# Performance work log

Measured on AMD Instinct MI355X. Metric: run time of the kernel, lower is better.

## Reference

```python
import jax, jax.numpy as jnp
import numpy as np

R, T, N, OPS = 3, 3, 50000, 24
E, B, MAXDEG = 400000, 32, 8
QD, ED, H = 128, 128, 128


def lstm_scan(x, Wih, Whh, bih, bhh):
    # x: (T, B, D). PyTorch LSTM gate order: i, f, g, o.
    Hh = Whh.shape[-1]
    def step(carry, xt):
        h, c = carry
        g = xt @ Wih.T + bih + h @ Whh.T + bhh
        i, f, gg, o = jnp.split(g, 4, axis=-1)
        c = jax.nn.sigmoid(f) * c + jax.nn.sigmoid(i) * jnp.tanh(gg)
        h = jax.nn.sigmoid(o) * jnp.tanh(c)
        return (h, c), h
    z = jnp.zeros((x.shape[1], Hh), x.dtype)
    (hT, _), ys = jax.lax.scan(step, (z, z), x)
    return ys, hT


def bilstm(x, Wih, Whh, bih, bhh):
    # weights have a leading direction axis of size 2 (fwd, bwd)
    ys_f, h_f = lstm_scan(x, Wih[0], Whh[0], bih[0], bhh[0])
    ys_b, h_b = lstm_scan(x[::-1], Wih[1], Whh[1], bih[1], bhh[1])
    return jnp.concatenate([ys_f, ys_b[::-1]], -1), jnp.concatenate([h_f, h_b], -1)


def setup_inputs() -> dict:
    key = jax.random.key(0)
    ks = jax.random.split(key, 20)
    s = 0.05
    inp = {}
    inp["queries"] = jax.random.randint(ks[0], (B,), 0, OPS)
    inp["heads"] = jax.random.randint(ks[1], (B,), 0, N)
    inp["rels"] = jax.random.randint(ks[2], (E,), 0, OPS // 2)
    inp["t_heads"] = jax.random.randint(ks[3], (E,), 0, N)
    inp["t_tails"] = jax.random.randint(ks[4], (E,), 0, N)
    inp["entity_degrees"] = jax.random.randint(ks[5], (N, MAXDEG), 0, OPS + 1)
    inp["query_embedding"] = jax.random.normal(ks[6], (OPS, QD)) * s
    ent = jax.random.normal(ks[7], (OPS + 1, ED)) * s
    inp["entity_embedding"] = ent.at[OPS].set(0.0)  # padding_idx row is zero
    inp["q_Wih"] = jax.random.normal(ks[8], (R, 2, 4 * H, QD)) * s
    inp["q_Whh"] = jax.random.normal(ks[9], (R, 2, 4 * H, H)) * s
    inp["q_bih"] = jax.random.normal(ks[10], (R, 2, 4 * H)) * s
    inp["q_bhh"] = jax.random.normal(ks[11], (R, 2, 4 * H)) * s
    inp["e_Wih"] = jax.random.normal(ks[12], (2, 4 * H, ED)) * s
    inp["e_Whh"] = jax.random.normal(ks[13], (2, 4 * H, H)) * s
    inp["e_bih"] = jax.random.normal(ks[14], (2, 4 * H)) * s
    inp["e_bhh"] = jax.random.normal(ks[15], (2, 4 * H)) * s
    inp["q_lin_W"] = jax.random.normal(ks[16], (OPS + 1, 2 * H)) * s
    inp["q_lin_b"] = jax.random.normal(ks[17], (OPS + 1,)) * s
    inp["e_lin_W"] = jax.random.normal(ks[18], (OPS, 2 * H)) * s
    inp["e_lin_b"] = jax.random.normal(ks[19], (OPS,)) * s
    return inp


def reference(queries, heads, rels, t_heads, t_tails, entity_degrees,
              query_embedding, entity_embedding, q_Wih, q_Whh, q_bih, q_bhh,
              e_Wih, e_Whh, e_bih, e_bhh, q_lin_W, q_lin_b, e_lin_W, e_lin_b):
    # --- query attention over operators, one BiLSTM per rank ---
    qx = jnp.broadcast_to(query_embedding[queries][None], (T, B, QD))  # (T, B, QD)
    def q_branch(Wih, Whh, bih, bhh):
        ys, _ = bilstm(qx, Wih, Whh, bih, bhh)                 # (T, B, 2H)
        return jax.nn.softmax(ys @ q_lin_W.T + q_lin_b, axis=-1)  # (T, B, OPS+1)
    query_attn = jax.vmap(q_branch)(q_Wih, q_Whh, q_bih, q_bhh)   # (R, T, B, OPS+1)

    # --- entity attention from degree-sequence BiLSTM (final hidden states) ---
    ex = entity_embedding[entity_degrees].transpose(1, 0, 2)      # (MAXDEG, N, ED)
    _, e_h = bilstm(ex, e_Wih, e_Whh, e_bih, e_bhh)               # (N, 2H)
    entity_attn = jax.nn.softmax(e_h @ e_lin_W.T + e_lin_b, axis=-1)  # (N, OPS)

    # sparse operator values: A_rel[h, t] = entity_attn[h, rel] for fact (rel, h, t)
    w = entity_attn[t_heads, rels]  # (E,)
    half = OPS // 2

    logits = jnp.zeros((B, N), jnp.float32)
    for r in range(R):
        memory = jax.nn.one_hot(heads, N, dtype=jnp.float32)  # (B, N)
        for t in range(T):
            qa = query_attn[r, t]  # (B, OPS+1)
            # forward op: (memory @ A_rel), weighted by qa[rel]
            fwd = (qa[:, rels] * w[None, :]) * memory[:, t_heads]        # (B, E)
            # reverse op: (memory @ A_rel.T), weighted by qa[rel + half]
            rev = (qa[:, rels + half] * w[None, :]) * memory[:, t_tails]  # (B, E)
            added = (jnp.zeros((B, N), jnp.float32)
                     .at[:, t_tails].add(fwd)
                     .at[:, t_heads].add(rev))
            added = added + memory * qa[:, -1:]
            memory = added / jnp.maximum(1e-20, added.sum(axis=1, keepdims=True))
        logits = logits + memory
    return logits
```

## Files before the change

### kernel.cpp

```cpp
#include <hip/hip_runtime.h>

#define R_ 3
#define T_ 3
#define N_ 50000
#define OPS_ 24
#define E_ 400000
#define B_ 32
#define MAXDEG_ 8
#define QD_ 128
#define ED_ 128
#define H_ 128
#define G4_ (4*H_)
#define HPAD 168
#define PSLOTS 64
#define RB_ 96

#define QB_ (R_ * B_)
#define WB_ ((2*32*5*64*8 + 511) / 512)
#define CB_ ((E_ + 511) / 512)
#define BF_ ((E_ + 511) / 512)
#define ZU_ 586
#define ZM_ 25
#define ZS_ 12
#define EB_ 16
#define SCANBLK_ ((N_ + 31) / 32)

typedef unsigned short u16;
typedef unsigned char u8;
typedef __attribute__((ext_vector_type(8))) short bf16x8;
typedef __attribute__((ext_vector_type(8))) _Float16 f16x8;
typedef __attribute__((ext_vector_type(4))) float f32x4;

#define BF16_ONE ((short)0x3F80)
#define LOG2E_  1.44269504f
#define LOG2E2_ 2.88539008f

__device__ __forceinline__ short f2bf(float f){
  union { float f; unsigned u; } v; v.f = f;
  unsigned r = v.u + 0x7fffu + ((v.u >> 16) & 1u);
  return (short)(r >> 16);
}
__device__ __forceinline__ float bf2f(u16 u){
  union { unsigned u; float f; } v; v.u = ((unsigned)u) << 16; return v.f;
}
__device__ __forceinline__ float frcp(float x){ return __builtin_amdgcn_rcpf(x); }
__device__ __forceinline__ float fsig(float x){ return frcp(1.0f + __expf(-x)); }
__device__ __forceinline__ float ftanh(float x){
  return __builtin_fmaf(2.0f, fsig(2.0f * x), -1.0f);
}
__device__ __forceinline__ float fexp2(float x){
#if __has_builtin(__builtin_amdgcn_exp2f)
  return __builtin_amdgcn_exp2f(x);
#else
  return __expf(x * 0.6931471806f);
#endif
}

__device__ void qattn_body(int bid, const int* __restrict__ queries, const float* __restrict__ qemb,
    const float* __restrict__ qWih, const float* __restrict__ qWhh,
    const float* __restrict__ qbih, const float* __restrict__ qbhh,
    const float* __restrict__ qlinW, const float* __restrict__ qlinb,
    float* __restrict__ query_attn )
{
  int r = bid / B_;
  int b = bid % B_;
  int tid = threadIdx.x;
  int d   = tid >> 8;
  int t2  = tid & 255;
  __shared__ float x[QD_];
  __shared__ float gx[2][G4_];
  __shared__ float h[2][H_], c[2][H_];
  __shared__ float gtmp[2][G4_];
  __shared__ float hh[2][T_][H_];
  __shared__ float lg[OPS_ + 1];

  int q = queries[b];
  if (tid < QD_) x[tid] = qemb[q * QD_ + tid];
  __syncthreads();

  const float* Wih = qWih + (size_t)(r * 2 + d) * G4_ * QD_;
  const float* Whh = qWhh + (size_t)(r * 2 + d) * G4_ * H_;
  const float* bih = qbih + (r * 2 + d) * G4_;
  const float* bhh = qbhh + (r * 2 + d) * G4_;
  for (int j = t2; j < G4_; j += 256){
    const float4* wr = (const float4*)(Wih + (size_t)j * QD_);
    float s = bih[j] + bhh[j];
    for (int k = 0; k < QD_ / 4; ++k){
      float4 wv = wr[k];
      s += wv.x * x[4*k] + wv.y * x[4*k+1] + wv.z * x[4*k+2] + wv.w * x[4*k+3];
    }
    gx[d][j] = s;
  }
  if (t2 < H_){ h[d][t2] = 0.f; c[d][t2] = 0.f; }
  __syncthreads();
  for (int t = 0; t < T_; ++t){
    for (int j = t2; j < G4_; j += 256){
      const float4* wr = (const float4*)(Whh + (size_t)j * H_);
      float s = 0.f;
      for (int k = 0; k < H_ / 4; ++k){
        float4 wv = wr[k];
        s += wv.x * h[d][4*k] + wv.y * h[d][4*k+1] + wv.z * h[d][4*k+2] + wv.w * h[d][4*k+3];
      }
      gtmp[d][j] = gx[d][j] + s;
    }
    __syncthreads();
    if (t2 < H_){
      float gi = gtmp[d][t2], gf = gtmp[d][t2 + H_], gg = gtmp[d][t2 + 2*H_], go = gtmp[d][t2 + 3*H_];
      float cn = fsig(gf) * c[d][t2] + fsig(gi) * ftanh(gg);
      float hn = fsig(go) * ftanh(cn);
      c[d][t2] = cn; h[d][t2] = hn;
      hh[d][t][t2] = hn;
    }
    __syncthreads();
  }

  for (int t = 0; t < T_; ++t){
    if (tid < OPS_ + 1){
      const float* wr = qlinW + tid * (2 * H_);
      float s = qlinb[tid];
      for (int k = 0; k < H_; ++k) s += wr[k] * hh[0][t][k];
      for (int k = 0; k < H_; ++k) s += wr[H_ + k] * hh[1][T_ - 1 - t][k];
      lg[tid] = s;
    }
    __syncthreads();
    if (tid == 0){
      float m = -1e30f;
      for (int o = 0; o < OPS_ + 1; ++o) m = fmaxf(m, lg[o]);
      float sum = 0.f;
      for (int o = 0; o < OPS_ + 1; ++o){ float e = __expf(lg[o] - m); lg[o] = e; sum += e; }
      float inv = frcp(sum);
      for (int o = 0; o < OPS_ + 1; ++o) lg[o] *= inv;
    }
    __syncthreads();
    if (tid < OPS_ + 1) query_attn[((size_t)(r * T_ + t) * B_ + b) * (OPS_ + 1) + tid] = lg[tid];
    __syncthreads();
  }
}

__device__ void wbuild_body(int bid, const float* __restrict__ eWhh,
                            const float* __restrict__ eemb, const float* __restrict__ eWih,
                            const float* __restrict__ ebih, const float* __restrict__ ebhh,
                            u16* __restrict__ wtile, u16* __restrict__ wonehot)
{
  int idx = bid * 512 + threadIdx.x;
  if (idx >= 2 * 32 * 5 * 64 * 8) return;
  int jj = idx & 7;
  int lane = (idx >> 3) & 63;
  int kc = (idx >> 9) % 5;
  int gtile = (idx / (8 * 64 * 5)) & 31;
  int dir = idx / (8 * 64 * 5 * 32);
  int row = lane >> 4, col = lane & 15;
  int j = gtile * 16 + col;
  float sc = ((gtile >> 3) == 2) ? LOG2E2_ : LOG2E_;
  if (kc < 4){
    int k = kc * 32 + row * 8 + jj;
    float v = eWhh[((size_t)dir * G4_ + j) * H_ + k] * sc;
    wtile[((((size_t)dir * 32 + gtile) * 4 + kc) * 64 + lane) * 8 + jj] = (u16)f2bf(v);
  } else {
    int vdeg = row * 8 + jj;
    float v = 0.f;
    if (vdeg <= OPS_){
      const float4* wr = (const float4*)(eWih + (size_t)(dir * G4_ + j) * ED_);
      const float4* er = (const float4*)(eemb + (size_t)vdeg * ED_);
      float s = ebih[dir * G4_ + j] + ebhh[dir * G4_ + j];
      for (int k = 0; k < ED_ / 4; ++k){
        float4 wv = wr[k], ev = er[k];
        s += wv.x * ev.x + wv.y * ev.y + wv.z * ev.z + wv.w * ev.w;
      }
      v = s * sc;
    }
    wonehot[(((size_t)dir * 32 + gtile) * 64 + lane) * 8 + jj] = (u16)f2bf(v);
  }
}

__device__ void csr_count_body(int bid, const int* __restrict__ theads,
                               const int* __restrict__ ttails, int* __restrict__ counts)
{
  int e = bid * 512 + threadIdx.x;
  if (e < E_){
    atomicAdd(&counts[ttails[e]], 1);
    atomicAdd(&counts[theads[e]], 1);
  }
}

__device__ void bfs1_body(int bid, const int* __restrict__ heads,
                          const int* __restrict__ theads, const int* __restrict__ ttails,
                          u8* __restrict__ hs1)
{
  if (bid == 0 && threadIdx.x < B_) hs1[heads[threadIdx.x]] = 1;
  int e = bid * 512 + threadIdx.x;
  if (e < E_){
    int a = theads[e], t = ttails[e];
    #pragma unroll 8
    for (int i = 0; i < B_; ++i){
      int hd = heads[i];
      if (a == hd) hs1[t] = 1;
      if (t == hd) hs1[a] = 1;
    }
  }
}

__global__ __launch_bounds__(512) void front_kernel(
    const int* queries, const float* qemb,
    const float* qWih, const float* qWhh, const float* qbih, const float* qbhh,
    const float* qlinW, const float* qlinb, float* query_attn,
    const float* eWhh, const float* eemb, const float* eWih,
    const float* ebih, const float* ebhh, u16* wtile, u16* wonehot,
    const int* theads, const int* ttails, int* counts,
    const int* heads, u8* hs1,
    float* u2, int* maski, float* sumsP,
    const float* elinW, u16* etile)
{
  int bid = blockIdx.x;
  int tid = threadIdx.x;
  if (bid < QB_){
    qattn_body(bid, queries, qemb, qWih, qWhh, qbih, qbhh, qlinW, qlinb, query_attn);
  } else if (bid < QB_ + WB_){
    wbuild_body(bid - QB_, eWhh, eemb, eWih, ebih, ebhh, wtile, wonehot);
  } else if (bid < QB_ + WB_ + CB_){
    csr_count_body(bid - QB_ - WB_, theads, ttails, counts);
  } else if (bid < QB_ + WB_ + CB_ + BF_){
    bfs1_body(bid - QB_ - WB_ - CB_, heads, theads, ttails, hs1);
  } else if (bid < QB_ + WB_ + CB_ + BF_ + ZU_){
    int zb = bid - QB_ - WB_ - CB_ - BF_;
    float4 z = {0.f, 0.f, 0.f, 0.f};
    size_t base = (size_t)zb * 8192 + tid * 4;
    #pragma unroll
    for (int k = 0; k < 4; ++k){
      size_t idx = base + (size_t)k * 2048;
      if (idx < (size_t)N_ * RB_) *(float4*)&u2[idx] = z;
    }
  } else if (bid < QB_ + WB_ + CB_ + BF_ + ZU_ + ZM_){
    int mi = (bid - QB_ - WB_ - CB_ - BF_ - ZU_) * 512 + tid;
    if (mi < (N_ + 3) / 4) maski[mi] = 0;
  } else if (bid < QB_ + WB_ + CB_ + BF_ + ZU_ + ZM_ + ZS_){
    int si = (bid - QB_ - WB_ - CB_ - BF_ - ZU_ - ZM_) * 512 + tid;
    if (si < PSLOTS * RB_) sumsP[si] = 0.f;
  } else {
    int idx = (bid - (QB_ + WB_ + CB_ + BF_ + ZU_ + ZM_ + ZS_)) * 512 + tid;
    if (idx < 8192){
      int jj = idx & 7;
      int lane = (idx >> 3) & 63;
      int ks = (idx >> 9) & 7;
      int ot = idx >> 12;
      int op = ot * 16 + (lane & 15);
      int k  = ks * 32 + (lane >> 4) * 8 + jj;
      float v = (op < OPS_) ? elinW[(size_t)op * (2 * H_) + k] : 0.f;
      _Float16 hv = (_Float16)v;
      etile[idx] = *(const u16*)&hv;
    }
  }
}

__global__ __launch_bounds__(512) void bfs2_kernel(
    const int* __restrict__ theads, const int* __restrict__ ttails,
    const u8* __restrict__ hs1, u8* __restrict__ mask)
{
  int bid = blockIdx.x;
  if (bid < BF_){
    int e = bid * 512 + threadIdx.x;
    if (e < E_){
      int a = theads[e], t = ttails[e];
      if (hs1[a]) mask[t] = 1;
      if (hs1[t]) mask[a] = 1;
    }
  } else {
    int n = (bid - BF_) * 512 + threadIdx.x;
    if (n < N_ && hs1[n]) mask[n] = 1;
  }
}

__device__ void scan_body(const int* __restrict__ counts, int* __restrict__ rowptr,
                          int* __restrict__ cursor, int* __restrict__ cursor2)
{
  __shared__ int wsum[8];
  int t = threadIdx.x;
  int lane = t & 63, wv = t >> 6;
  int carry = 0;
  for (int base = 0; base < N_; base += 2048){
    int idx = base + t * 4;
    int c0 = 0, c1 = 0, c2 = 0, c3 = 0;
    if (idx + 3 < N_){
      int4 c = *(const int4*)&counts[idx];
      c0 = c.x; c1 = c.y; c2 = c.z; c3 = c.w;
    } else {
      if (idx     < N_) c0 = counts[idx];
      if (idx + 1 < N_) c1 = counts[idx + 1];
      if (idx + 2 < N_) c2 = counts[idx + 2];
      if (idx + 3 < N_) c3 = counts[idx + 3];
    }
    int s = c0 + c1 + c2 + c3;
    int sc = s;
    #pragma unroll
    for (int off = 1; off < 64; off <<= 1){
      int v = __shfl_up(sc, off);
      if (lane >= off) sc += v;
    }
    if (lane == 63) wsum[wv] = sc;
    __syncthreads();
    if (t == 0){
      int acc = carry;
      #pragma unroll
      for (int w = 0; w < 8; ++w){ int v = wsum[w]; wsum[w] = acc; acc += v; }
      carry = acc;
    }
    __syncthreads();
    int excl = wsum[wv] + (sc - s);
    int r0 = excl, r1 = r0 + c0, r2 = r1 + c1, r3 = r2 + c2;
    if (idx + 3 < N_){
      int4 rv; rv.x = r0; rv.y = r1; rv.z = r2; rv.w = r3;
      *(int4*)&rowptr[idx]  = rv;
      *(int4*)&cursor[idx]  = rv;
      *(int4*)&cursor2[idx] = rv;
    } else {
      if (idx     < N_){ rowptr[idx]   = r0; cursor[idx]   = r0; cursor2[idx]   = r0; }
      if (idx + 1 < N_){ rowptr[idx+1] = r1; cursor[idx+1] = r1; cursor2[idx+1] = r1; }
      if (idx + 2 < N_){ rowptr[idx+2] = r2; cursor[idx+2] = r2; cursor2[idx+2] = r2; }
      if (idx + 3 < N_){ rowptr[idx+3] = r3; cursor[idx+3] = r3; cursor2[idx+3] = r3; }
    }
  }
  if (t == 0) rowptr[N_] = carry;
}

__global__ __launch_bounds__(512, 4) void elstm_kernel(
    const int* __restrict__ degs,
    const u16* __restrict__ wtile, const u16* __restrict__ wonehot,
    const u16* __restrict__ etile, const float* __restrict__ elinb,
    float* __restrict__ attn ,
    const int* __restrict__ counts, int* __restrict__ rowptr,
    int* __restrict__ cursor, int* __restrict__ cursor2)
{
  if (blockIdx.x == 0){ scan_body(counts, rowptr, cursor, cursor2); return; }

  int tid = threadIdx.x;
  int lane = tid & 63;
  int w = tid >> 6;
  int wu = __builtin_amdgcn_readfirstlane(w);
  int row = lane >> 4, col = lane & 15;
  int ebase = (blockIdx.x - 1) * 32;

  __shared__ __align__(16) short hl[2][32 * HPAD];
  __shared__ __align__(16) short hfin[32 * 136];
  __shared__ float lgs[32][33];

  int eg0 = ebase + tid; if (eg0 >= N_) eg0 = N_ - 1;

  for (int i = tid; i < 2 * 32 * HPAD; i += 512) ((short*)hl)[i] = 0;
  __syncthreads();
  if (tid < 32) hl[0][tid * HPAD + H_ + degs[(size_t)eg0 * MAXDEG_ + 0]] = BF16_ONE;
  __syncthreads();

  int swzr = (col >> 2) & 3;

  for (int dir = 0; dir < 2; ++dir){
    const u16* Wt  = wtile   + (size_t)dir * 32 * 4 * 64 * 8;
    const u16* Woh = wonehot + (size_t)dir * 32 * 64 * 8;
    const u16* W0 = Wt + (size_t)((0 * 8 + wu) * 4 * 64) * 8;
    const u16* W1 = Wt + (size_t)((1 * 8 + wu) * 4 * 64) * 8;
    const u16* W2 = Wt + (size_t)((2 * 8 + wu) * 4 * 64) * 8;
    const u16* W3 = Wt + (size_t)((3 * 8 + wu) * 4 * 64) * 8;
    const u16* O0 = Woh + (size_t)((0 * 8 + wu) * 64) * 8;
    const u16* O1 = Woh + (size_t)((1 * 8 + wu) * 64) * 8;
    const u16* O2 = Woh + (size_t)((2 * 8 + wu) * 64) * 8;
    const u16* O3 = Woh + (size_t)((3 * 8 + wu) * 64) * 8;
    float cst[8];
    #pragma unroll
    for (int i = 0; i < 8; ++i) cst[i] = 0.f;

    for (int t = 0; t < MAXDEG_; ++t){
      const short* hb = hl[t & 1];
      short*       hw = hl[(t + 1) & 1];
      f32x4 acc[8];
      #pragma unroll
      for (int i = 0; i < 8; ++i) acc[i] = (f32x4){0.f, 0.f, 0.f, 0.f};

      #pragma unroll 2
      for (int kc = 0; kc < 4; ++kc){
        bf16x8 af0 = *(const bf16x8*)&hb[(col) * HPAD + kc * 32 + (row ^ swzr) * 8];
        bf16x8 af1 = *(const bf16x8*)&hb[(16 + col) * HPAD + kc * 32 + (row ^ swzr) * 8];
        int lo = (kc * 64 + lane) * 8;
        bf16x8 b0 = *(const bf16x8*)(W0 + lo);
        bf16x8 b1 = *(const bf16x8*)(W1 + lo);
        bf16x8 b2 = *(const bf16x8*)(W2 + lo);
        bf16x8 b3 = *(const bf16x8*)(W3 + lo);
        acc[0] = __builtin_amdgcn_mfma_f32_16x16x32_bf16(af0, b0, acc[0], 0, 0, 0);
        acc[1] = __builtin_amdgcn_mfma_f32_16x16x32_bf16(af1, b0, acc[1], 0, 0, 0);
        acc[2] = __builtin_amdgcn_mfma_f32_16x16x32_bf16(af0, b1, acc[2], 0, 0, 0);
        acc[3] = __builtin_amdgcn_mfma_f32_16x16x32_bf16(af1, b1, acc[3], 0, 0, 0);
        acc[4] = __builtin_amdgcn_mfma_f32_16x16x32_bf16(af0, b2, acc[4], 0, 0, 0);
        acc[5] = __builtin_amdgcn_mfma_f32_16x16x32_bf16(af1, b2, acc[5], 0, 0, 0);
        acc[6] = __builtin_amdgcn_mfma_f32_16x16x32_bf16(af0, b3, acc[6], 0, 0, 0);
        acc[7] = __builtin_amdgcn_mfma_f32_16x16x32_bf16(af1, b3, acc[7], 0, 0, 0);
      }
      {
        bf16x8 af0 = *(const bf16x8*)&hb[(col) * HPAD + H_ + row * 8];
        bf16x8 af1 = *(const bf16x8*)&hb[(16 + col) * HPAD + H_ + row * 8];
        int lo = lane * 8;
        bf16x8 b0 = *(const bf16x8*)(O0 + lo);
        bf16x8 b1 = *(const bf16x8*)(O1 + lo);
        bf16x8 b2 = *(const bf16x8*)(O2 + lo);
        bf16x8 b3 = *(const bf16x8*)(O3 + lo);
        acc[0] = __builtin_amdgcn_mfma_f32_16x16x32_bf16(af0, b0, acc[0], 0, 0, 0);
        acc[1] = __builtin_amdgcn_mfma_f32_16x16x32_bf16(af1, b0, acc[1], 0, 0, 0);
        acc[2] = __builtin_amdgcn_mfma_f32_16x16x32_bf16(af0, b1, acc[2], 0, 0, 0);
        acc[3] = __builtin_amdgcn_mfma_f32_16x16x32_bf16(af1, b1, acc[3], 0, 0, 0);
        acc[4] = __builtin_amdgcn_mfma_f32_16x16x32_bf16(af0, b2, acc[4], 0, 0, 0);
        acc[5] = __builtin_amdgcn_mfma_f32_16x16x32_bf16(af1, b2, acc[5], 0, 0, 0);
        acc[6] = __builtin_amdgcn_mfma_f32_16x16x32_bf16(af0, b3, acc[6], 0, 0, 0);
        acc[7] = __builtin_amdgcn_mfma_f32_16x16x32_bf16(af1, b3, acc[7], 0, 0, 0);
      }

      #pragma unroll
      for (int mt = 0; mt < 2; ++mt){
        #pragma unroll
        for (int reg = 0; reg < 4; ++reg){
          int e = mt * 16 + row * 4 + reg;
          int jsw = (((wu * 2 + (col >> 3)) ^ row) * 8) + (col & 7);
          float Gi = acc[0 + mt][reg];
          float Gf = acc[2 + mt][reg];
          float Gg = acc[4 + mt][reg];
          float Go = acc[6 + mt][reg];
          int ci = mt * 4 + reg;
          float ea = fexp2(-Gi);
          float ef = fexp2(-Gf);
          float eb = fexp2(-Gg);
          float eo = fexp2(-Go);
          float t1 = 1.f + ef, t2 = 1.f + ea, t3 = 1.f + eb;
          float p = t2 * t3;
          float num = __builtin_fmaf(cst[ci], p, (1.f - eb) * t1);
          float cn = num * frcp(t1 * p);
          float ed = fexp2(cn * (-LOG2E2_));
          float hn = (1.f - ed) * frcp((1.f + eo) * (1.f + ed));
          cst[ci] = cn;
          hw[e * HPAD + jsw] = f2bf(hn);
        }
      }
      if (tid < 32){
        const int* dr = degs + (size_t)eg0 * MAXDEG_;
        if (t >= 1)
          hw[tid * HPAD + H_ + dr[dir ? (MAXDEG_ - t) : (t - 1)]] = 0;
        if (t < MAXDEG_ - 1)
          hw[tid * HPAD + H_ + dr[dir ? (MAXDEG_ - 2 - t) : (t + 1)]] = BF16_ONE;
      }
      __syncthreads();
    }

    if (dir == 0){
      for (int i = tid; i < 32 * 16; i += 512){
        int e = i >> 4, c = i & 15;
        int sz = (e >> 2) & 3;
        *(bf16x8*)&hfin[e * 136 + c * 8] =
            *(const bf16x8*)&hl[0][e * HPAD + ((c ^ sz) * 8)];
      }
      __syncthreads();
      for (int i = tid; i < 2 * 32 * HPAD; i += 512) ((short*)hl)[i] = 0;
      __syncthreads();
      if (tid < 32) hl[0][tid * HPAD + H_ + degs[(size_t)eg0 * MAXDEG_ + (MAXDEG_ - 1)]] = BF16_ONE;
      __syncthreads();
    }
  }

  if (wu < 4){
    int mt = wu >> 1, ot = wu & 1;
    int e2 = mt * 16 + col;
    f32x4 accL = (f32x4){0.f, 0.f, 0.f, 0.f};
    #pragma unroll
    for (int ks = 0; ks < 8; ++ks){
      bf16x8 ra;
      if (ks < 4) ra = *(const bf16x8*)&hfin[e2 * 136 + ks * 32 + row * 8];
      else        ra = *(const bf16x8*)&hl[0][e2 * HPAD + (ks - 4) * 32 + (row ^ swzr) * 8];
      f16x8 af;
      #pragma unroll
      for (int jj = 0; jj < 8; ++jj) af[jj] = (_Float16)bf2f((u16)ra[jj]);
      f16x8 bfr = *(const f16x8*)(etile + (((size_t)(ot * 8 + ks)) * 64 + lane) * 8);
      accL = __builtin_amdgcn_mfma_f32_16x16x32_f16(af, bfr, accL, 0, 0, 0);
    }
    #pragma unroll
    for (int reg = 0; reg < 4; ++reg){
      int ent = mt * 16 + (lane >> 4) * 4 + reg;
      int op  = ot * 16 + (lane & 15);
      float bb = (op < OPS_) ? elinb[op] : 0.f;
      lgs[ent][op] = accL[reg] + bb;
    }
  }
  __syncthreads();
  if (tid < 32){
    int n = ebase + tid;
    if (n < N_){
      float m = -1e30f;
      #pragma unroll
      for (int o = 0; o < OPS_; ++o) m = fmaxf(m, lgs[tid][o]);
      float s = 0.f;
      #pragma unroll
      for (int o = 0; o < OPS_; ++o) s += __expf(lgs[tid][o] - m);
      float inv = frcp(s);
      #pragma unroll
      for (int o = 0; o < OPS_; ++o)
        attn[(size_t)n * OPS_ + o] = __expf(lgs[tid][o] - m) * inv;
    }
  }
}

__global__ void csr_fill_kernel(const int* __restrict__ rels, const int* __restrict__ theads,
                                const int* __restrict__ ttails, const float* __restrict__ attn,
                                const u8* __restrict__ mask, const u8* __restrict__ hs1,
                                int* __restrict__ cursor, int* __restrict__ cursor2,
                                uint2* __restrict__ ents, uint2* __restrict__ ents2)
{
  int e = blockIdx.x * 256 + threadIdx.x;
  if (e < E_){
    int hh = theads[e], tt = ttails[e];
    int mh = mask[hh], mt = mask[tt];
    if (!(mh | mt)) return;
    int rel = rels[e];
    unsigned wb = __float_as_uint(attn[(size_t)hh * OPS_ + rel]);
    if (mh){
      uint2 v1; v1.x = (unsigned)hh | ((unsigned)rel << 16); v1.y = wb;
      ents[atomicAdd(&cursor[tt], 1)] = v1;
    }
    if (mt){
      uint2 v2; v2.x = (unsigned)tt | ((unsigned)(rel + OPS_/2) << 16); v2.y = wb;
      ents[atomicAdd(&cursor[hh], 1)] = v2;
    }
    if (hs1[hh]){
      uint2 w1; w1.x = (unsigned)tt | ((unsigned)rel << 16); w1.y = wb;
      ents2[atomicAdd(&cursor2[hh], 1)] = w1;
    }
    if (hs1[tt]){
      uint2 w2; w2.x = (unsigned)hh | ((unsigned)(rel + OPS_/2) << 16); w2.y = wb;
      ents2[atomicAdd(&cursor2[tt], 1)] = w2;
    }
  }
}

__global__ void t01_kernel(const int* __restrict__ heads, const float* __restrict__ query_attn,
                           const int* __restrict__ rowptr, const int* __restrict__ cend2,
                           const uint2* __restrict__ ents2, float* __restrict__ u2)
{
  __shared__ float qa0[OPS_ + 1], qa1[OPS_ + 1];
  int blk = blockIdx.x;
  int r = blk >> 5, b = blk & 31;
  int rb = r * 32 + b;
  int tid = threadIdx.x;
  if (tid < OPS_ + 1){
    qa0[tid] = query_attn[((size_t)(r * T_ + 0) * B_ + b) * (OPS_ + 1) + tid];
    qa1[tid] = query_attn[((size_t)(r * T_ + 1) * B_ + b) * (OPS_ + 1) + tid];
  }
  __syncthreads();
  int hd = heads[b];
  int beg = rowptr[hd], end = cend2[hd];
  float q024 = qa0[OPS_], q124 = qa1[OPS_];
  if (tid == 0) atomicAdd(&u2[(size_t)hd * RB_ + rb], q124 * q024);
  for (int i = beg + tid; i < end; i += 64){
    uint2 e1 = ents2[i];
    int s  = (int)(e1.x & 0xFFFFu);
    int r1 = (int)(e1.x >> 16);
    float w1 = __uint_as_float(e1.y);
    atomicAdd(&u2[(size_t)s * RB_ + rb], w1 * (q124 * qa0[r1] + qa1[r1] * q024));
    float v1 = qa0[r1] * w1;
    int b2 = rowptr[s], e2e = cend2[s];
    for (int jj = b2; jj < e2e; ++jj){
      uint2 e2 = ents2[jj];
      int d2 = (int)(e2.x & 0xFFFFu);
      int r2 = (int)(e2.x >> 16);
      atomicAdd(&u2[(size_t)d2 * RB_ + rb], qa1[r2] * __uint_as_float(e2.y) * v1);
    }
  }
}

__global__ __launch_bounds__(256) void gather3_kernel(
    const float* __restrict__ ucur, float* __restrict__ unxt,
    const float* __restrict__ query_attn, int t,
    const int* __restrict__ rowptr, const int* __restrict__ cend,
    const uint2* __restrict__ ents, const u8* __restrict__ mask,
    float* __restrict__ partial )
{
  __shared__ float qas[3 * B_ * (OPS_ + 1)];
  __shared__ float red[RB_];
  int tid = threadIdx.x;
  for (int i = tid; i < 3 * B_ * (OPS_ + 1); i += 256){
    int r = i / (B_ * (OPS_ + 1));
    int rem = i - r * (B_ * (OPS_ + 1));
    qas[i] = query_attn[(size_t)(r * T_ + t) * B_ * (OPS_ + 1) + rem];
  }
  if (tid < RB_) red[tid] = 0.f;
  __syncthreads();
  int b  = tid & 31;
  int h  = (tid >> 5) & 1;
  int n = blockIdx.x * 4 + (tid >> 6);
  const float* q0 = &qas[0 * 800 + b * (OPS_ + 1)];
  const float* q1 = &qas[1 * 800 + b * (OPS_ + 1)];
  const float* q2 = &qas[2 * 800 + b * (OPS_ + 1)];
  size_t nb = (size_t)n * RB_;
  float a0 = 0.f, a1 = 0.f, a2 = 0.f;
  if (h == 0 && mask[n]){
    a0 = ucur[nb + b]      * q0[OPS_];
    a1 = ucur[nb + 32 + b] * q1[OPS_];
    a2 = ucur[nb + 64 + b] * q2[OPS_];
  }
  int beg = rowptr[n], end = cend[n];
  int cnt = end - beg;
  int nq = cnt >> 2;
  for (int c = h; c < nq; c += 2){
    int i0 = beg + 4 * c;
    uint2 e0 = ents[i0 + 0];
    uint2 e1 = ents[i0 + 1];
    uint2 e2 = ents[i0 + 2];
    uint2 e3 = ents[i0 + 3];
    size_t s0 = (size_t)(e0.x & 0xFFFFu) * RB_;
    size_t s1 = (size_t)(e1.x & 0xFFFFu) * RB_;
    size_t s2 = (size_t)(e2.x & 0xFFFFu) * RB_;
    size_t s3 = (size_t)(e3.x & 0xFFFFu) * RB_;
    float u00 = ucur[s0 + b], u01 = ucur[s0 + 32 + b], u02 = ucur[s0 + 64 + b];
    float u10 = ucur[s1 + b], u11 = ucur[s1 + 32 + b], u12 = ucur[s1 + 64 + b];
    float u20 = ucur[s2 + b], u21 = ucur[s2 + 32 + b], u22 = ucur[s2 + 64 + b];
    float u30 = ucur[s3 + b], u31 = ucur[s3 + 32 + b], u32 = ucur[s3 + 64 + b];
    int r0 = (int)(e0.x >> 16), r1 = (int)(e1.x >> 16);
    int r2 = (int)(e2.x >> 16), r3 = (int)(e3.x >> 16);
    float w0 = __uint_as_float(e0.y), w1 = __uint_as_float(e1.y);
    float w2 = __uint_as_float(e2.y), w3 = __uint_as_float(e3.y);
    a0 += q0[r0]*w0*u00 + q0[r1]*w1*u10 + q0[r2]*w2*u20 + q0[r3]*w3*u30;
    a1 += q1[r0]*w0*u01 + q1[r1]*w1*u11 + q1[r2]*w2*u21 + q1[r3]*w3*u31;
    a2 += q2[r0]*w0*u02 + q2[r1]*w1*u12 + q2[r2]*w2*u22 + q2[r3]*w3*u32;
  }
  if (h == 1){
    for (int i = beg + 4 * nq; i < end; ++i){
      uint2 e0 = ents[i];
      size_t s0 = (size_t)(e0.x & 0xFFFFu) * RB_;
      int r0 = (int)(e0.x >> 16);
      float w0 = __uint_as_float(e0.y);
      a0 += q0[r0] * w0 * ucur[s0 + b];
      a1 += q1[r0] * w0 * ucur[s0 + 32 + b];
      a2 += q2[r0] * w0 * ucur[s0 + 64 + b];
    }
  }
  a0 += __shfl_xor(a0, 32);
  a1 += __shfl_xor(a1, 32);
  a2 += __shfl_xor(a2, 32);
  if (h == 0){
    unxt[nb + b]      = a0;
    unxt[nb + 32 + b] = a1;
    unxt[nb + 64 + b] = a2;
    atomicAdd(&red[b], a0);
    atomicAdd(&red[32 + b], a1);
    atomicAdd(&red[64 + b], a2);
  }
  __syncthreads();
  if (tid < RB_)
    atomicAdd(&partial[(blockIdx.x & (PSLOTS - 1)) * RB_ + tid], red[tid]);
}

__global__ void fintrans_kernel(const float* __restrict__ u, const float* __restrict__ partial,
                                float* __restrict__ out)
{
  __shared__ float sinv[RB_];
  __shared__ float t[B_][72];
  int tid = threadIdx.x;
  if (tid < RB_){
    float s = 0.f;
    #pragma unroll 8
    for (int k = 0; k < PSLOTS; ++k) s += partial[k * RB_ + tid];
    sinv[tid] = frcp(fmaxf(1e-20f, s));
  }
  __syncthreads();
  int n0 = blockIdx.x * 64;
  for (int i = tid; i < 64 * B_; i += 256){
    int nl = i >> 5, b = i & 31;
    int n = n0 + nl;
    float v = 0.f;
    if (n < N_){
      size_t nb = (size_t)n * RB_;
      v = u[nb + b] * sinv[b] + u[nb + 32 + b] * sinv[32 + b] + u[nb + 64 + b] * sinv[64 + b];
    }
    t[b][nl] = v;
  }
  __syncthreads();
  for (int i = tid; i < 64 * B_; i += 256){
    int b = i >> 6, nl = i & 63;
    int n = n0 + nl;
    if (n < N_) out[(size_t)b * N_ + n] = t[b][nl];
  }
}

extern "C" void kernel_launch(void* const* d_in, const int* in_sizes, int n_in,
                              void* d_out, int out_size, void* d_ws, size_t ws_size,
                              hipStream_t stream)
{
  const int*   queries = (const int*)d_in[0];
  const int*   heads   = (const int*)d_in[1];
  const int*   rels    = (const int*)d_in[2];
  const int*   t_heads = (const int*)d_in[3];
  const int*   t_tails = (const int*)d_in[4];
  const int*   edeg    = (const int*)d_in[5];
  const float* qemb    = (const float*)d_in[6];
  const float* eemb    = (const float*)d_in[7];
  const float* qWih    = (const float*)d_in[8];
  const float* qWhh    = (const float*)d_in[9];
  const float* qbih    = (const float*)d_in[10];
  const float* qbhh    = (const float*)d_in[11];
  const float* eWih    = (const float*)d_in[12];
  const float* eWhh    = (const float*)d_in[13];
  const float* ebih    = (const float*)d_in[14];
  const float* ebhh    = (const float*)d_in[15];
  const float* qlinW   = (const float*)d_in[16];
  const float* qlinb   = (const float*)d_in[17];
  const float* elinW   = (const float*)d_in[18];
  const float* elinb   = (const float*)d_in[19];
  float* out = (float*)d_out;

  char* ws = (char*)d_ws;
  size_t off = 0;
  auto alloc = [&](size_t bytes){ void* p = ws + off; off += (bytes + 255) & ~(size_t)255; return p; };
  char*  bigB  = (char*)alloc((size_t)N_ * RB_ * 4);
  float* attn  = (float*)bigB;
  float* u3    = (float*)bigB;
  uint2* ents       = (uint2*)alloc((size_t)2 * E_ * 8);
  float* u2         = (float*)alloc((size_t)N_ * RB_ * 4);
  uint2* ents2      = (uint2*)alloc((size_t)2 * E_ * 8);
  float* query_attn = (float*)alloc((size_t)R_ * T_ * B_ * (OPS_ + 1) * 4);
  u16*   wtile      = (u16*)  alloc((size_t)2 * 32 * 4 * 64 * 8 * 2);
  u16*   wonehot    = (u16*)  alloc((size_t)2 * 32 * 64 * 8 * 2);
  u16*   etile      = (u16*)  alloc((size_t)2 * 8 * 64 * 8 * 2);
  int*   counts     = (int*)  alloc((size_t)(N_ + 1) * 4);
  int*   rowptr     = (int*)  alloc((size_t)(N_ + 1) * 4);
  int*   cursor     = (int*)  alloc((size_t)(N_ + 1) * 4);
  int*   cursor2    = (int*)  alloc((size_t)(N_ + 1) * 4);
  u8*    hs1        = (u8*)   alloc((size_t)N_);
  u8*    mask       = (u8*)   alloc((size_t)N_);
  float* sumsP      = (float*)alloc((size_t)PSLOTS * RB_ * 4);

  hipMemsetAsync(counts, 0, (size_t)(N_ + 1) * 4, stream);
  hipMemsetAsync(hs1, 0, (size_t)N_, stream);

  front_kernel<<<QB_ + WB_ + CB_ + BF_ + ZU_ + ZM_ + ZS_ + EB_, 512, 0, stream>>>(
      queries, qemb, qWih, qWhh, qbih, qbhh, qlinW, qlinb, query_attn,
      eWhh, eemb, eWih, ebih, ebhh, wtile, wonehot,
      t_heads, t_tails, counts, heads, hs1, u2, (int*)mask, sumsP, elinW, etile);
  bfs2_kernel<<<BF_ + (N_ + 511) / 512, 512, 0, stream>>>(t_heads, t_tails, hs1, mask);
  elstm_kernel<<<SCANBLK_ + 1, 512, 0, stream>>>(edeg, wtile, wonehot, etile, elinb,
                                                 attn, counts, rowptr, cursor, cursor2);
  csr_fill_kernel<<<(E_ + 255) / 256, 256, 0, stream>>>(rels, t_heads, t_tails, attn,
                                                        mask, hs1, cursor, cursor2,
                                                        ents, ents2);
  t01_kernel<<<RB_, 64, 0, stream>>>(heads, query_attn, rowptr, cursor2, ents2, u2);
  gather3_kernel<<<N_ / 4, 256, 0, stream>>>(u2, u3, query_attn, 2, rowptr, cursor,
                                             ents, mask, sumsP);
  fintrans_kernel<<<(N_ + 63) / 64, 256, 0, stream>>>(u3, sumsP, out);
}
```

Before: 463.2 us.

## Fold bfs2 and query-attention blocks into elstm launch; skip empty gather nodes

Removes the separate bfs2 launch and moves the query-attention LSTM blocks out of front_kernel into extra blocks of elstm_kernel alongside the scan block. This cuts one kernel launch and shortens front_kernel's critical path. gather3 now lets whole blocks exit early when all four nodes have no edges and no mask bit, and it skips writing their u3 values. fintrans reads zero for those nodes instead of the unwritten u3. The price is a block-wide sync before the shared-memory load and extra index reads in fintrans.

```diff
diff --git a/kernel.cpp b/kernel.cpp
--- a/kernel.cpp
+++ b/kernel.cpp
@@ -15,7 +15,6 @@
 #define PSLOTS 64
 #define RB_ 96
 
-#define QB_ (R_ * B_)
 #define WB_ ((2*32*5*64*8 + 511) / 512)
 #define CB_ ((E_ + 511) / 512)
 #define BF_ ((E_ + 511) / 512)
@@ -23,6 +22,11 @@
 #define ZM_ 25
 #define ZS_ 12
 #define EB_ 16
+
+#define QB_ (R_ * B_)
+#define BF2E_ ((E_ + 511) / 512)
+#define BF2N_ ((N_ + 511) / 512)
+#define RIDERS_ (1 + BF2E_ + BF2N_ + QB_)
 #define SCANBLK_ ((N_ + 31) / 32)
 
 typedef unsigned short u16;
@@ -201,9 +205,6 @@
 }
 
 __global__ __launch_bounds__(512) void front_kernel(
-    const int* queries, const float* qemb,
-    const float* qWih, const float* qWhh, const float* qbih, const float* qbhh,
-    const float* qlinW, const float* qlinb, float* query_attn,
     const float* eWhh, const float* eemb, const float* eWih,
     const float* ebih, const float* ebhh, u16* wtile, u16* wonehot,
     const int* theads, const int* ttails, int* counts,
@@ -213,16 +214,14 @@
 {
   int bid = blockIdx.x;
   int tid = threadIdx.x;
-  if (bid < QB_){
-    qattn_body(bid, queries, qemb, qWih, qWhh, qbih, qbhh, qlinW, qlinb, query_attn);
-  } else if (bid < QB_ + WB_){
-    wbuild_body(bid - QB_, eWhh, eemb, eWih, ebih, ebhh, wtile, wonehot);
-  } else if (bid < QB_ + WB_ + CB_){
-    csr_count_body(bid - QB_ - WB_, theads, ttails, counts);
-  } else if (bid < QB_ + WB_ + CB_ + BF_){
-    bfs1_body(bid - QB_ - WB_ - CB_, heads, theads, ttails, hs1);
-  } else if (bid < QB_ + WB_ + CB_ + BF_ + ZU_){
-    int zb = bid - QB_ - WB_ - CB_ - BF_;
+  if (bid < WB_){
+    wbuild_body(bid, eWhh, eemb, eWih, ebih, ebhh, wtile, wonehot);
+  } else if (bid < WB_ + CB_){
+    csr_count_body(bid - WB_, theads, ttails, counts);
+  } else if (bid < WB_ + CB_ + BF_){
+    bfs1_body(bid - WB_ - CB_, heads, theads, ttails, hs1);
+  } else if (bid < WB_ + CB_ + BF_ + ZU_){
+    int zb = bid - WB_ - CB_ - BF_;
     float4 z = {0.f, 0.f, 0.f, 0.f};
     size_t base = (size_t)zb * 8192 + tid * 4;
     #pragma unroll
@@ -230,14 +229,14 @@
       size_t idx = base + (size_t)k * 2048;
       if (idx < (size_t)N_ * RB_) *(float4*)&u2[idx] = z;
     }
-  } else if (bid < QB_ + WB_ + CB_ + BF_ + ZU_ + ZM_){
-    int mi = (bid - QB_ - WB_ - CB_ - BF_ - ZU_) * 512 + tid;
+  } else if (bid < WB_ + CB_ + BF_ + ZU_ + ZM_){
+    int mi = (bid - WB_ - CB_ - BF_ - ZU_) * 512 + tid;
     if (mi < (N_ + 3) / 4) maski[mi] = 0;
-  } else if (bid < QB_ + WB_ + CB_ + BF_ + ZU_ + ZM_ + ZS_){
-    int si = (bid - QB_ - WB_ - CB_ - BF_ - ZU_ - ZM_) * 512 + tid;
+  } else if (bid < WB_ + CB_ + BF_ + ZU_ + ZM_ + ZS_){
+    int si = (bid - WB_ - CB_ - BF_ - ZU_ - ZM_) * 512 + tid;
     if (si < PSLOTS * RB_) sumsP[si] = 0.f;
   } else {
-    int idx = (bid - (QB_ + WB_ + CB_ + BF_ + ZU_ + ZM_ + ZS_)) * 512 + tid;
+    int idx = (bid - (WB_ + CB_ + BF_ + ZU_ + ZM_ + ZS_)) * 512 + tid;
     if (idx < 8192){
       int jj = idx & 7;
       int lane = (idx >> 3) & 63;
@@ -252,12 +251,11 @@
   }
 }
 
-__global__ __launch_bounds__(512) void bfs2_kernel(
-    const int* __restrict__ theads, const int* __restrict__ ttails,
-    const u8* __restrict__ hs1, u8* __restrict__ mask)
-{
-  int bid = blockIdx.x;
-  if (bid < BF_){
+__device__ void bfs2_body(int bid, const int* __restrict__ theads,
+                          const int* __restrict__ ttails,
+                          const u8* __restrict__ hs1, u8* __restrict__ mask)
+{
+  if (bid < BF2E_){
     int e = bid * 512 + threadIdx.x;
     if (e < E_){
       int a = theads[e], t = ttails[e];
@@ -265,7 +263,7 @@
       if (hs1[t]) mask[a] = 1;
     }
   } else {
-    int n = (bid - BF_) * 512 + threadIdx.x;
+    int n = (bid - BF2E_) * 512 + threadIdx.x;
     if (n < N_ && hs1[n]) mask[n] = 1;
   }
 }
@@ -328,16 +326,30 @@
     const u16* __restrict__ etile, const float* __restrict__ elinb,
     float* __restrict__ attn ,
     const int* __restrict__ counts, int* __restrict__ rowptr,
-    int* __restrict__ cursor, int* __restrict__ cursor2)
-{
-  if (blockIdx.x == 0){ scan_body(counts, rowptr, cursor, cursor2); return; }
+    int* __restrict__ cursor, int* __restrict__ cursor2,
+    const int* __restrict__ theads, const int* __restrict__ ttails,
+    const u8* __restrict__ hs1, u8* __restrict__ mask,
+    const int* __restrict__ queries, const float* __restrict__ qemb,
+    const float* __restrict__ qWih, const float* __restrict__ qWhh,
+    const float* __restrict__ qbih, const float* __restrict__ qbhh,
+    const float* __restrict__ qlinW, const float* __restrict__ qlinb,
+    float* __restrict__ query_attn)
+{
+  int bid = blockIdx.x;
+  if (bid == 0){ scan_body(counts, rowptr, cursor, cursor2); return; }
+  if (bid < 1 + BF2E_ + BF2N_){ bfs2_body(bid - 1, theads, ttails, hs1, mask); return; }
+  if (bid < RIDERS_){
+    qattn_body(bid - (1 + BF2E_ + BF2N_), queries, qemb, qWih, qWhh, qbih, qbhh,
+               qlinW, qlinb, query_attn);
+    return;
+  }
 
   int tid = threadIdx.x;
   int lane = tid & 63;
   int w = tid >> 6;
   int wu = __builtin_amdgcn_readfirstlane(w);
   int row = lane >> 4, col = lane & 15;
-  int ebase = (blockIdx.x - 1) * 32;
+  int ebase = (bid - RIDERS_) * 32;
 
   __shared__ __align__(16) short hl[2][32 * HPAD];
   __shared__ __align__(16) short hfin[32 * 136];
@@ -578,6 +590,14 @@
   __shared__ float qas[3 * B_ * (OPS_ + 1)];
   __shared__ float red[RB_];
   int tid = threadIdx.x;
+  int b  = tid & 31;
+  int h  = (tid >> 5) & 1;
+  int n = blockIdx.x * 4 + (tid >> 6);
+  int beg = rowptr[n], end = cend[n];
+  int mk = mask[n];
+  int cnt = end - beg;
+  if (__syncthreads_and(cnt == 0 && !mk)) return;
+
   for (int i = tid; i < 3 * B_ * (OPS_ + 1); i += 256){
     int r = i / (B_ * (OPS_ + 1));
     int rem = i - r * (B_ * (OPS_ + 1));
@@ -585,21 +605,16 @@
   }
   if (tid < RB_) red[tid] = 0.f;
   __syncthreads();
-  int b  = tid & 31;
-  int h  = (tid >> 5) & 1;
-  int n = blockIdx.x * 4 + (tid >> 6);
   const float* q0 = &qas[0 * 800 + b * (OPS_ + 1)];
   const float* q1 = &qas[1 * 800 + b * (OPS_ + 1)];
   const float* q2 = &qas[2 * 800 + b * (OPS_ + 1)];
   size_t nb = (size_t)n * RB_;
   float a0 = 0.f, a1 = 0.f, a2 = 0.f;
-  if (h == 0 && mask[n]){
+  if (h == 0 && mk){
     a0 = ucur[nb + b]      * q0[OPS_];
     a1 = ucur[nb + 32 + b] * q1[OPS_];
     a2 = ucur[nb + 64 + b] * q2[OPS_];
   }
-  int beg = rowptr[n], end = cend[n];
-  int cnt = end - beg;
   int nq = cnt >> 2;
   for (int c = h; c < nq; c += 2){
     int i0 = beg + 4 * c;
@@ -637,7 +652,7 @@
   a0 += __shfl_xor(a0, 32);
   a1 += __shfl_xor(a1, 32);
   a2 += __shfl_xor(a2, 32);
-  if (h == 0){
+  if (h == 0 && (mk || cnt > 0)){
     unxt[nb + b]      = a0;
     unxt[nb + 32 + b] = a1;
     unxt[nb + 64 + b] = a2;
@@ -651,6 +666,8 @@
 }
 
 __global__ void fintrans_kernel(const float* __restrict__ u, const float* __restrict__ partial,
+                                const int* __restrict__ rowptr, const int* __restrict__ cend,
+                                const u8* __restrict__ mask,
                                 float* __restrict__ out)
 {
   __shared__ float sinv[RB_];
@@ -668,7 +685,7 @@
     int nl = i >> 5, b = i & 31;
     int n = n0 + nl;
     float v = 0.f;
-    if (n < N_){
+    if (n < N_ && (mask[n] || cend[n] > rowptr[n])){
       size_t nb = (size_t)n * RB_;
       v = u[nb + b] * sinv[b] + u[nb + 32 + b] * sinv[32 + b] + u[nb + 64 + b] * sinv[64 + b];
     }
@@ -732,18 +749,20 @@
   hipMemsetAsync(counts, 0, (size_t)(N_ + 1) * 4, stream);
   hipMemsetAsync(hs1, 0, (size_t)N_, stream);
 
-  front_kernel<<<QB_ + WB_ + CB_ + BF_ + ZU_ + ZM_ + ZS_ + EB_, 512, 0, stream>>>(
-      queries, qemb, qWih, qWhh, qbih, qbhh, qlinW, qlinb, query_attn,
+  front_kernel<<<WB_ + CB_ + BF_ + ZU_ + ZM_ + ZS_ + EB_, 512, 0, stream>>>(
       eWhh, eemb, eWih, ebih, ebhh, wtile, wonehot,
       t_heads, t_tails, counts, heads, hs1, u2, (int*)mask, sumsP, elinW, etile);
-  bfs2_kernel<<<BF_ + (N_ + 511) / 512, 512, 0, stream>>>(t_heads, t_tails, hs1, mask);
-  elstm_kernel<<<SCANBLK_ + 1, 512, 0, stream>>>(edeg, wtile, wonehot, etile, elinb,
-                                                 attn, counts, rowptr, cursor, cursor2);
+  elstm_kernel<<<RIDERS_ + SCANBLK_, 512, 0, stream>>>(
+      edeg, wtile, wonehot, etile, elinb, attn,
+      counts, rowptr, cursor, cursor2,
+      t_heads, t_tails, hs1, mask,
+      queries, qemb, qWih, qWhh, qbih, qbhh, qlinW, qlinb, query_attn);
   csr_fill_kernel<<<(E_ + 255) / 256, 256, 0, stream>>>(rels, t_heads, t_tails, attn,
                                                         mask, hs1, cursor, cursor2,
                                                         ents, ents2);
   t01_kernel<<<RB_, 64, 0, stream>>>(heads, query_attn, rowptr, cursor2, ents2, u2);
   gather3_kernel<<<N_ / 4, 256, 0, stream>>>(u2, u3, query_attn, 2, rowptr, cursor,
                                              ents, mask, sumsP);
-  fintrans_kernel<<<(N_ + 63) / 64, 256, 0, stream>>>(u3, sumsP, out);
-}
+  fintrans_kernel<<<(N_ + 63) / 64, 256, 0, stream>>>(u3, sumsP, rowptr, cursor,
+                                                      mask, out);
+}
```

New measurement: 450.3 us. 1.03x faster.
